# Optimization experiments

Measured on AMD Instinct MI355X. Metric: run time of the kernel, lower is better.

## Reference

```python
import jax, jax.numpy as jnp
import numpy as np

CH = 512
GROUPS = 32  # _valid_num_groups(512, 32)
EPS = 1e-6

def setup_inputs() -> dict:
    key = jax.random.key(0)
    ks = jax.random.split(key, 11)
    B, C, H, W = 8, CH, 64, 64
    s = 0.02
    return {
        "x": jax.random.normal(ks[0], (B, C, H, W), jnp.float32),
        "gn_w": jnp.ones((C,), jnp.float32),
        "gn_b": jnp.zeros((C,), jnp.float32),
        "q_w": jax.random.normal(ks[1], (C, C), jnp.float32) * s,
        "q_b": jnp.zeros((C,), jnp.float32),
        "k_w": jax.random.normal(ks[2], (C, C), jnp.float32) * s,
        "k_b": jnp.zeros((C,), jnp.float32),
        "v_w": jax.random.normal(ks[3], (C, C), jnp.float32) * s,
        "v_b": jnp.zeros((C,), jnp.float32),
        "proj_w": jax.random.normal(ks[4], (C, C), jnp.float32) * s,
        "proj_b": jnp.zeros((C,), jnp.float32),
    }

def _group_norm(x, w, b):
    B, C, H, W = x.shape
    g = GROUPS
    xg = x.reshape(B, g, C // g, H, W)
    mu = xg.mean(axis=(2, 3, 4), keepdims=True)
    var = xg.var(axis=(2, 3, 4), keepdims=True)
    xn = ((xg - mu) * jax.lax.rsqrt(var + EPS)).reshape(B, C, H, W)
    return xn * w[None, :, None, None] + b[None, :, None, None]

def _conv1x1(h, w, b):
    # h: [B,C,H,W]; w: [Cout,Cin]; 1x1 conv == channel matmul
    return jnp.einsum('bchw,dc->bdhw', h, w) + b[None, :, None, None]

def reference(x, gn_w, gn_b, q_w, q_b, k_w, k_b, v_w, v_b, proj_w, proj_b):
    B, C, H, W = x.shape
    N = H * W
    h = _group_norm(x, gn_w, gn_b)
    q = _conv1x1(h, q_w, q_b).reshape(B, C, N)  # [B,C,N]
    k = _conv1x1(h, k_w, k_b).reshape(B, C, N)
    v = _conv1x1(h, v_w, v_b).reshape(B, C, N)
    # attn[b,i,j] = sum_c q[b,c,i]*k[b,c,j] scaled
    attn = jnp.einsum('bci,bcj->bij', q, k) * (C ** -0.5)
    attn = jax.nn.softmax(attn, axis=-1)
    # out[b,c,i] = sum_j v[b,c,j]*attn[b,i,j]  (bmm(v, attn^T))
    o = jnp.einsum('bcj,bij->bci', v, attn).reshape(B, C, H, W)
    o = _conv1x1(o, proj_w, proj_b)
    return x + o
```

## Files before the change

kernel.cpp:

```cpp
#include <hip/hip_runtime.h>

typedef unsigned short u16;
typedef __attribute__((ext_vector_type(8))) short short8;
typedef __attribute__((ext_vector_type(4))) float f32x4;

__device__ __forceinline__ u16 f32_to_bf16(float f) {
  unsigned u = __float_as_uint(f);
  u += 0x7fffu + ((u >> 16) & 1u);
  return (u16)(u >> 16);
}
__device__ __forceinline__ float bf16_to_f32(u16 h) {
  return __uint_as_float(((unsigned)h) << 16);
}

#define GLD_LDS16(gp, lp)                                                  \
  __builtin_amdgcn_global_load_lds(                                        \
      (const __attribute__((address_space(1))) void*)(gp),                 \
      (__attribute__((address_space(3))) void*)(lp), 16, 0, 0)

__global__ __launch_bounds__(256) void cvt4_f32_bf16(const float* __restrict__ s0,
                                                     const float* __restrict__ s1,
                                                     const float* __restrict__ s2,
                                                     const float* __restrict__ s3,
                                                     u16* __restrict__ d0,
                                                     u16* __restrict__ d1,
                                                     u16* __restrict__ d2,
                                                     u16* __restrict__ d3) {
  const float* s = blockIdx.y == 0 ? s0 : blockIdx.y == 1 ? s1 : blockIdx.y == 2 ? s2 : s3;
  u16* d = blockIdx.y == 0 ? d0 : blockIdx.y == 1 ? d1 : blockIdx.y == 2 ? d2 : d3;
  int i = blockIdx.x * 256 + threadIdx.x;
  float4 v = ((const float4*)s)[i];
  uint2 r;
  r.x = (unsigned)f32_to_bf16(v.x) | ((unsigned)f32_to_bf16(v.y) << 16);
  r.y = (unsigned)f32_to_bf16(v.z) | ((unsigned)f32_to_bf16(v.w) << 16);
  ((uint2*)d)[i] = r;
}

__global__ __launch_bounds__(1024) void gn_stats(const float* __restrict__ x,
                                                 float2* __restrict__ stats) {
  int bg = blockIdx.x;
  const float* xp = x + (long)bg * 65536;
  int t = threadIdx.x;
  float s = 0.f, ss = 0.f;
  for (int i = t; i < 16384; i += 1024) {
    float4 v = ((const float4*)xp)[i];
    s += (v.x + v.y) + (v.z + v.w);
    ss += (v.x * v.x + v.y * v.y) + (v.z * v.z + v.w * v.w);
  }
#pragma unroll
  for (int o = 32; o; o >>= 1) { s += __shfl_xor(s, o); ss += __shfl_xor(ss, o); }
  __shared__ float rs[16], rq[16];
  int wave = t >> 6, lane = t & 63;
  if (lane == 0) { rs[wave] = s; rq[wave] = ss; }
  __syncthreads();
  if (wave == 0) {
    float a = lane < 16 ? rs[lane] : 0.f;
    float b = lane < 16 ? rq[lane] : 0.f;
#pragma unroll
    for (int o = 8; o; o >>= 1) { a += __shfl_xor(a, o); b += __shfl_xor(b, o); }
    if (lane == 0) {
      float mean = a * (1.f / 65536.f);
      float var = b * (1.f / 65536.f) - mean * mean;
      stats[bg] = make_float2(mean, rsqrtf(var + 1e-6f));
    }
  }
}

__global__ __launch_bounds__(256) void gn_apply_t(const float* __restrict__ x,
                                                  const float* __restrict__ gw,
                                                  const float* __restrict__ gb,
                                                  const float2* __restrict__ stats,
                                                  u16* __restrict__ hT) {
  const int g = blockIdx.y, bb = blockIdx.z;
  const float2 st = stats[bb * 32 + g];
  const float mean = st.x, rstd = st.y;
  const float* xp = x + ((long)bb * 512 + g * 16) * 4096;
  u16* hp = hT + (long)bb * 4096 * 512 + g * 16;
  const int i = blockIdx.x * 1024 + threadIdx.x * 4;
#pragma unroll
  for (int half = 0; half < 2; ++half) {
    float w[8], bv[8];
#pragma unroll
    for (int c = 0; c < 8; ++c) {
      w[c] = gw[g * 16 + half * 8 + c] * rstd;
      bv[c] = gb[g * 16 + half * 8 + c];
    }
    float v[8][4];
#pragma unroll
    for (int c = 0; c < 8; ++c) {
      float4 f = *(const float4*)(xp + (long)(half * 8 + c) * 4096 + i);
      v[c][0] = f.x; v[c][1] = f.y; v[c][2] = f.z; v[c][3] = f.w;
    }
#pragma unroll
    for (int p = 0; p < 4; ++p) {
      u16 o[8];
#pragma unroll
      for (int c = 0; c < 8; ++c) o[c] = f32_to_bf16((v[c][p] - mean) * w[c] + bv[c]);
      *(int4*)(hp + (long)(i + p) * 512 + half * 8) = *(int4*)o;
    }
  }
}

template <int EPI>
__global__ __launch_bounds__(256) void gemm128(
    const u16* __restrict__ Ab, long sA, int lda,
    const u16* __restrict__ Bb, long sB, int ldb,
    void* __restrict__ Cb, long sC, int ldc,
    const float* __restrict__ biasM, const float* __restrict__ biasN,
    float scale, const float* __restrict__ res, long sR, int K) {
  const u16* A = Ab + (long)blockIdx.z * sA;
  const u16* B = Bb + (long)blockIdx.z * sB;
  const int m0 = blockIdx.y * 128, n0 = blockIdx.x * 128;
  const int t = threadIdx.x;
  const int wave = t >> 6, lane = t & 63;
  const int wy = wave >> 1, wx = wave & 1;
  const int lr = lane & 15, q = lane >> 4;
  __shared__ __align__(16) u16 As[128 * 32];
  __shared__ __align__(16) u16 Bs[128 * 32];
  f32x4 acc[4][4] = {};
  for (int k0 = 0; k0 < K; k0 += 32) {
#pragma unroll
    for (int c = 0; c < 2; ++c) {
      const int chunk = c * 256 + t;
      const int row = chunk >> 2, ko = (chunk & 3) << 3;
      const int ldsoff = (c * 256 + wave * 64) * 8;
      GLD_LDS16(A + (long)(m0 + row) * lda + (k0 + ko), As + ldsoff);
      GLD_LDS16(B + (long)(n0 + row) * ldb + (k0 + ko), Bs + ldsoff);
    }
    __syncthreads();
    short8 af[4], bf[4];
#pragma unroll
    for (int i = 0; i < 4; ++i)
      af[i] = *(const short8*)(&As[(wy * 64 + i * 16 + lr) * 32 + q * 8]);
#pragma unroll
    for (int j = 0; j < 4; ++j)
      bf[j] = *(const short8*)(&Bs[(wx * 64 + j * 16 + lr) * 32 + q * 8]);
#pragma unroll
    for (int i = 0; i < 4; ++i)
#pragma unroll
      for (int j = 0; j < 4; ++j)
        acc[i][j] = __builtin_amdgcn_mfma_f32_16x16x32_bf16(af[i], bf[j], acc[i][j], 0, 0, 0);
    __syncthreads();
  }
#pragma unroll
  for (int i = 0; i < 4; ++i) {
#pragma unroll
    for (int r = 0; r < 4; ++r) {
      const int mr = m0 + wy * 64 + i * 16 + q * 4 + r;
      const float bm = biasM ? biasM[mr] : 0.f;
#pragma unroll
      for (int j = 0; j < 4; ++j) {
        const int nc = n0 + wx * 64 + j * 16 + lr;
        float vv = acc[i][j][r] + bm;
        if (biasN) vv += biasN[nc];
        vv *= scale;
        const long off = (long)blockIdx.z * sC + (long)mr * ldc + nc;
        if (EPI == 0) {
          ((u16*)Cb)[off] = f32_to_bf16(vv);
        } else {
          ((float*)Cb)[off] = vv + res[(long)blockIdx.z * sR + (long)mr * ldc + nc];
        }
      }
    }
  }
}

__global__ __launch_bounds__(256) void softmax_kernel(u16* __restrict__ P) {
  u16* pr = P + (long)blockIdx.y * 4096 * 4096 + (long)blockIdx.x * 4096;
  int t = threadIdx.x;
  int lane = t & 63, wave = t >> 6;
  int4 d0 = ((const int4*)pr)[t];
  int4 d1 = ((const int4*)pr)[t + 256];
  const u16* p0 = (const u16*)&d0;
  const u16* p1 = (const u16*)&d1;
  float v[16];
#pragma unroll
  for (int j = 0; j < 8; ++j) { v[j] = bf16_to_f32(p0[j]); v[8 + j] = bf16_to_f32(p1[j]); }
  float mx = v[0];
#pragma unroll
  for (int j = 1; j < 16; ++j) mx = fmaxf(mx, v[j]);
#pragma unroll
  for (int o = 32; o; o >>= 1) mx = fmaxf(mx, __shfl_xor(mx, o));
  __shared__ float sm[4];
  __shared__ float ssum[4];
  if (lane == 0) sm[wave] = mx;
  __syncthreads();
  mx = fmaxf(fmaxf(sm[0], sm[1]), fmaxf(sm[2], sm[3]));
  float s = 0.f;
#pragma unroll
  for (int j = 0; j < 16; ++j) { v[j] = __expf(v[j] - mx); s += v[j]; }
#pragma unroll
  for (int o = 32; o; o >>= 1) s += __shfl_xor(s, o);
  if (lane == 0) ssum[wave] = s;
  __syncthreads();
  s = ssum[0] + ssum[1] + ssum[2] + ssum[3];
  float inv = 1.0f / s;
  unsigned r0[4], r1[4];
#pragma unroll
  for (int j = 0; j < 4; ++j) {
    r0[j] = (unsigned)f32_to_bf16(v[2 * j] * inv) | ((unsigned)f32_to_bf16(v[2 * j + 1] * inv) << 16);
    r1[j] = (unsigned)f32_to_bf16(v[8 + 2 * j] * inv) | ((unsigned)f32_to_bf16(v[8 + 2 * j + 1] * inv) << 16);
  }
  ((int4*)pr)[t] = *(int4*)r0;
  ((int4*)pr)[t + 256] = *(int4*)r1;
}

extern "C" void kernel_launch(void* const* d_in, const int* in_sizes, int n_in,
                              void* d_out, int out_size, void* d_ws, size_t ws_size,
                              hipStream_t stream) {
  const float* x = (const float*)d_in[0];
  const float* gn_w = (const float*)d_in[1];
  const float* gn_b = (const float*)d_in[2];
  const float* q_w = (const float*)d_in[3];
  const float* q_b = (const float*)d_in[4];
  const float* k_w = (const float*)d_in[5];
  const float* k_b = (const float*)d_in[6];
  const float* v_w = (const float*)d_in[7];
  const float* v_b = (const float*)d_in[8];
  const float* p_w = (const float*)d_in[9];
  const float* p_b = (const float*)d_in[10];

  char* ws = (char*)d_ws;
  const size_t MB = 1ull << 20;
  u16* wqb = (u16*)(ws + 0);
  u16* wkb = (u16*)(ws + 512 * 1024);
  u16* wvb = (u16*)(ws + 1 * MB);
  u16* wpb = (u16*)(ws + 3 * MB / 2);
  u16* hb = (u16*)(ws + 2 * MB);
  u16* vb = (u16*)(ws + 34 * MB);
  u16* Pb = (u16*)(ws + 66 * MB);
  float2* stats = (float2*)(ws + 66 * MB);
  u16* qb = (u16*)d_out;
  u16* kb = (u16*)d_out + 512L * 4096 * 8;
  u16* ob = hb;

  int NB = 1;
  if (ws_size >= 66 * MB + 8 * 32 * MB) NB = 8;
  else if (ws_size >= 66 * MB + 4 * 32 * MB) NB = 4;
  else if (ws_size >= 66 * MB + 2 * 32 * MB) NB = 2;

  cvt4_f32_bf16<<<dim3(256, 4), 256, 0, stream>>>(q_w, k_w, v_w, p_w, wqb, wkb, wvb, wpb);
  gn_stats<<<256, 1024, 0, stream>>>(x, stats);
  gn_apply_t<<<dim3(4, 32, 8), 256, 0, stream>>>(x, gn_w, gn_b, stats, hb);

  const long sCN = 512L * 4096;
  const long sNN = 4096L * 4096;
  const float scale = 0.04419417382415922f;

  gemm128<0><<<dim3(4, 32, 8), 256, 0, stream>>>(
      hb, sCN, 512, wqb, 0, 512, qb, sCN, 512, nullptr, q_b, scale, nullptr, 0, 512);
  gemm128<0><<<dim3(4, 32, 8), 256, 0, stream>>>(
      hb, sCN, 512, wkb, 0, 512, kb, sCN, 512, nullptr, k_b, 1.0f, nullptr, 0, 512);
  gemm128<0><<<dim3(32, 4, 8), 256, 0, stream>>>(
      wvb, 0, 512, hb, sCN, 512, vb, sCN, 4096, v_b, nullptr, 1.0f, nullptr, 0, 512);

  for (int b0 = 0; b0 < 8; b0 += NB) {
    gemm128<0><<<dim3(32, 32, NB), 256, 0, stream>>>(
        qb + b0 * sCN, sCN, 512, kb + b0 * sCN, sCN, 512, Pb, sNN, 4096,
        nullptr, nullptr, 1.0f, nullptr, 0, 512);
    softmax_kernel<<<dim3(4096, NB), 256, 0, stream>>>(Pb);
    gemm128<0><<<dim3(4, 32, NB), 256, 0, stream>>>(
        Pb, sNN, 4096, vb + b0 * sCN, sCN, 4096, ob + b0 * sCN, sCN, 512,
        nullptr, nullptr, 1.0f, nullptr, 0, 4096);
  }

  gemm128<1><<<dim3(32, 4, 8), 256, 0, stream>>>(
      wpb, 0, 512, ob, sCN, 512, (float*)d_out, sCN, 4096, p_b, nullptr, 1.0f,
      x, sCN, 512);
}
```

Before: 971.5 us.

## Stage bf16 GEMM epilogue through LDS and swizzle PV blocks across XCDs

For bf16-output GEMMs, the accumulator tile is written to padded shared memory and then stored to global memory as coalesced 16-byte rows, replacing scattered 2-byte stores. The P·V GEMM now uses a 1D grid with an XCD-aware remap. Blocks that share the same row-slab of P land on the same XCD, so its L2 serves the reuse of the large P matrix. This costs an extra LDS round-trip and barrier in the epilogue, and shared memory grows to 34 KB, which may lower occupancy.

```diff
diff --git a/kernel.cpp b/kernel.cpp
--- a/kernel.cpp
+++ b/kernel.cpp
@@ -101,22 +101,34 @@
   }
 }
 
-template <int EPI>
+template <int EPI, bool SWZ>
 __global__ __launch_bounds__(256) void gemm128(
     const u16* __restrict__ Ab, long sA, int lda,
     const u16* __restrict__ Bb, long sB, int ldb,
     void* __restrict__ Cb, long sC, int ldc,
     const float* __restrict__ biasM, const float* __restrict__ biasN,
     float scale, const float* __restrict__ res, long sR, int K) {
-  const u16* A = Ab + (long)blockIdx.z * sA;
-  const u16* B = Bb + (long)blockIdx.z * sB;
-  const int m0 = blockIdx.y * 128, n0 = blockIdx.x * 128;
+  int bx, by, bz;
+  if (SWZ) {
+    const int lid = blockIdx.x;
+    const int xcd = lid & 7, s = lid >> 3;
+    bx = s & 3;
+    const int rest = s >> 2;
+    by = xcd + 8 * (rest & 3);
+    bz = rest >> 2;
+  } else {
+    bx = blockIdx.x; by = blockIdx.y; bz = blockIdx.z;
+  }
+  const u16* A = Ab + (long)bz * sA;
+  const u16* B = Bb + (long)bz * sB;
+  const int m0 = by * 128, n0 = bx * 128;
   const int t = threadIdx.x;
   const int wave = t >> 6, lane = t & 63;
   const int wy = wave >> 1, wx = wave & 1;
   const int lr = lane & 15, q = lane >> 4;
-  __shared__ __align__(16) u16 As[128 * 32];
-  __shared__ __align__(16) u16 Bs[128 * 32];
+  __shared__ __align__(16) char smem[34816];
+  u16* As = (u16*)smem;
+  u16* Bs = As + 128 * 32;
   f32x4 acc[4][4] = {};
   for (int k0 = 0; k0 < K; k0 += 32) {
 #pragma unroll
@@ -142,23 +154,42 @@
         acc[i][j] = __builtin_amdgcn_mfma_f32_16x16x32_bf16(af[i], bf[j], acc[i][j], 0, 0, 0);
     __syncthreads();
   }
-#pragma unroll
-  for (int i = 0; i < 4; ++i) {
-#pragma unroll
-    for (int r = 0; r < 4; ++r) {
-      const int mr = m0 + wy * 64 + i * 16 + q * 4 + r;
-      const float bm = biasM ? biasM[mr] : 0.f;
-#pragma unroll
-      for (int j = 0; j < 4; ++j) {
-        const int nc = n0 + wx * 64 + j * 16 + lr;
-        float vv = acc[i][j][r] + bm;
-        if (biasN) vv += biasN[nc];
-        vv *= scale;
-        const long off = (long)blockIdx.z * sC + (long)mr * ldc + nc;
-        if (EPI == 0) {
-          ((u16*)Cb)[off] = f32_to_bf16(vv);
-        } else {
-          ((float*)Cb)[off] = vv + res[(long)blockIdx.z * sR + (long)mr * ldc + nc];
+  if (EPI == 0) {
+    u16* Cs = (u16*)smem;
+#pragma unroll
+    for (int i = 0; i < 4; ++i) {
+#pragma unroll
+      for (int r = 0; r < 4; ++r) {
+        const int ml = wy * 64 + i * 16 + q * 4 + r;
+        const float bm = biasM ? biasM[m0 + ml] : 0.f;
+#pragma unroll
+        for (int j = 0; j < 4; ++j) {
+          const int nl = wx * 64 + j * 16 + lr;
+          float vv = acc[i][j][r] + bm;
+          if (biasN) vv += biasN[n0 + nl];
+          Cs[ml * 136 + nl] = f32_to_bf16(vv * scale);
+        }
+      }
+    }
+    __syncthreads();
+    const int row = t >> 1, cb = (t & 1) * 64;
+    u16* gout = (u16*)Cb + (long)bz * sC + (long)(m0 + row) * ldc + n0 + cb;
+    const u16* ls = Cs + row * 136 + cb;
+#pragma unroll
+    for (int u = 0; u < 8; ++u) ((int4*)gout)[u] = *(const int4*)(ls + u * 8);
+  } else {
+#pragma unroll
+    for (int i = 0; i < 4; ++i) {
+#pragma unroll
+      for (int r = 0; r < 4; ++r) {
+        const int mr = m0 + wy * 64 + i * 16 + q * 4 + r;
+        const float bm = biasM ? biasM[mr] : 0.f;
+#pragma unroll
+        for (int j = 0; j < 4; ++j) {
+          const int nc = n0 + wx * 64 + j * 16 + lr;
+          float vv = (acc[i][j][r] + bm) * scale;
+          const long off = (long)bz * sC + (long)mr * ldc + nc;
+          ((float*)Cb)[off] = vv + res[(long)bz * sR + (long)mr * ldc + nc];
         }
       }
     }
@@ -247,24 +278,24 @@
   const long sNN = 4096L * 4096;
   const float scale = 0.04419417382415922f;
 
-  gemm128<0><<<dim3(4, 32, 8), 256, 0, stream>>>(
+  gemm128<0, false><<<dim3(4, 32, 8), 256, 0, stream>>>(
       hb, sCN, 512, wqb, 0, 512, qb, sCN, 512, nullptr, q_b, scale, nullptr, 0, 512);
-  gemm128<0><<<dim3(4, 32, 8), 256, 0, stream>>>(
+  gemm128<0, false><<<dim3(4, 32, 8), 256, 0, stream>>>(
       hb, sCN, 512, wkb, 0, 512, kb, sCN, 512, nullptr, k_b, 1.0f, nullptr, 0, 512);
-  gemm128<0><<<dim3(32, 4, 8), 256, 0, stream>>>(
+  gemm128<0, false><<<dim3(32, 4, 8), 256, 0, stream>>>(
       wvb, 0, 512, hb, sCN, 512, vb, sCN, 4096, v_b, nullptr, 1.0f, nullptr, 0, 512);
 
   for (int b0 = 0; b0 < 8; b0 += NB) {
-    gemm128<0><<<dim3(32, 32, NB), 256, 0, stream>>>(
+    gemm128<0, false><<<dim3(32, 32, NB), 256, 0, stream>>>(
         qb + b0 * sCN, sCN, 512, kb + b0 * sCN, sCN, 512, Pb, sNN, 4096,
         nullptr, nullptr, 1.0f, nullptr, 0, 512);
     softmax_kernel<<<dim3(4096, NB), 256, 0, stream>>>(Pb);
-    gemm128<0><<<dim3(4, 32, NB), 256, 0, stream>>>(
+    gemm128<0, true><<<128 * NB, 256, 0, stream>>>(
         Pb, sNN, 4096, vb + b0 * sCN, sCN, 4096, ob + b0 * sCN, sCN, 512,
         nullptr, nullptr, 1.0f, nullptr, 0, 4096);
   }
 
-  gemm128<1><<<dim3(32, 4, 8), 256, 0, stream>>>(
+  gemm128<1, false><<<dim3(32, 4, 8), 256, 0, stream>>>(
       wpb, 0, 512, ob, sCN, 512, (float*)d_out, sCN, 4096, p_b, nullptr, 1.0f,
       x, sCN, 512);
 }
```

Measured after the change: 988.3 us. No clear change (+1.7%).
